# Performance work log

Hardware: AMD Instinct MI355X
Metric: run time of the kernel (lower is better)

## Reference

```python
import jax, jax.numpy as jnp
import numpy as np

B, S, H = 1, 4096, 2048
NH, HD = 16, 128
ROPE_N = 32
WINDOW = 1024
EPS = 1e-5


def _build_rope(seq_len, n_elem, base=10000.0):
    theta = 1.0 / (base ** (np.arange(0, n_elem, 2, dtype=np.float32) / n_elem))  # [n_elem/2]
    idx = np.arange(seq_len, dtype=np.float32)
    freqs = np.outer(idx, theta)                     # [S, n_elem/2]
    freqs = np.concatenate([freqs, freqs], axis=-1)  # [S, n_elem]
    return jnp.asarray(np.cos(freqs)), jnp.asarray(np.sin(freqs))


def setup_inputs() -> dict:
    key = jax.random.key(0)
    k1, k2, k3 = jax.random.split(key, 3)
    x = jax.random.normal(k1, (B, S, H), dtype=jnp.float32)
    cos, sin = _build_rope(S, ROPE_N)
    norm_weight = jnp.ones((H,), dtype=jnp.float32)
    qkv_w = jax.random.normal(k2, (3 * H, H), dtype=jnp.float32) * (1.0 / np.sqrt(H))
    o_w = jax.random.normal(k3, (H, H), dtype=jnp.float32) * (1.0 / np.sqrt(H))
    return {"x": x, "cos": cos, "sin": sin, "norm_weight": norm_weight,
            "qkv_w": qkv_w, "o_w": o_w}


def _apply_rope(t, cos, sin):
    # t: [B, NH, S, ROPE_N]; cos/sin: [S, ROPE_N]
    half = t.shape[-1] // 2
    x1, x2 = t[..., :half], t[..., half:]
    rotated = jnp.concatenate([-x2, x1], axis=-1)
    return t * cos + rotated * sin


def reference(x, cos, sin, norm_weight, qkv_w, o_w):
    b, s, h = x.shape
    # RMSNorm (computed in fp32)
    xf = x.astype(jnp.float32)
    ms = jnp.mean(xf * xf, axis=-1, keepdims=True)
    xn = (norm_weight * (xf * jax.lax.rsqrt(ms + EPS))).astype(x.dtype)
    # fused QKV projection
    qkv = jnp.einsum('bsh,oh->bso', xn, qkv_w)  # [B, S, 3H]
    q, k, v = jnp.split(qkv, 3, axis=-1)
    def to_heads(t):
        return t.reshape(b, s, NH, HD).transpose(0, 2, 1, 3)  # [B, NH, S, HD]
    q, k, v = to_heads(q), to_heads(k), to_heads(v)
    # partial RoPE on first ROPE_N dims
    q = jnp.concatenate([_apply_rope(q[..., :ROPE_N], cos, sin), q[..., ROPE_N:]], axis=-1)
    k = jnp.concatenate([_apply_rope(k[..., :ROPE_N], cos, sin), k[..., ROPE_N:]], axis=-1)
    # sliding-window causal attention: query i attends keys j with i-WINDOW <= j <= i
    scale = 1.0 / np.sqrt(HD)
    scores = jnp.einsum('bnqd,bnkd->bnqk', q, k) * scale  # [B, NH, S, S]
    i = jnp.arange(s)[:, None]
    j = jnp.arange(s)[None, :]
    mask = (j <= i) & (j >= i - WINDOW)
    scores = jnp.where(mask, scores, jnp.finfo(scores.dtype).min)
    attn = jax.nn.softmax(scores, axis=-1)
    out = jnp.einsum('bnqk,bnkd->bnqd', attn, v)  # [B, NH, S, HD]
    out = out.transpose(0, 2, 1, 3).reshape(b, s, h)
    return jnp.einsum('bsh,oh->bso', out, o_w)
```

## Files before the change

### kernel.cpp

```cpp
#include <hip/hip_runtime.h>
#include <stdint.h>

#define S_LEN 4096
#define HDIM  2048
#define NHEAD 16
#define HD    128
#define WIN   1024

typedef float  f32x4  __attribute__((ext_vector_type(4)));
typedef float  f32x4v __attribute__((ext_vector_type(4)));
typedef __bf16 bf16x8 __attribute__((ext_vector_type(8)));
typedef short  short8 __attribute__((ext_vector_type(8)));
typedef short  short4v __attribute__((ext_vector_type(4)));

static __device__ __forceinline__ short f2bf(float f) {
  union { float f; uint32_t u; } v; v.f = f;
  uint32_t r = (v.u + 0x7FFFu + ((v.u >> 16) & 1u)) >> 16;
  return (short)(uint16_t)r;
}

static __device__ __forceinline__ void gload_lds16(const void* g, void* l) {
  __builtin_amdgcn_global_load_lds((__attribute__((address_space(1))) void*)g,
                                   (__attribute__((address_space(3))) void*)l,
                                   16, 0, 0);
}

__global__ __launch_bounds__(256) void rmsnorm_k(const float* __restrict__ x,
                                                 const float* __restrict__ w,
                                                 short* __restrict__ xn) {
  const int row = blockIdx.x;
  const int t = threadIdx.x;
  const float* xr = x + (size_t)row * HDIM;
  f32x4v a = *(const f32x4v*)&xr[t * 8];
  f32x4v b = *(const f32x4v*)&xr[t * 8 + 4];
  float ss = a.x*a.x + a.y*a.y + a.z*a.z + a.w*a.w
           + b.x*b.x + b.y*b.y + b.z*b.z + b.w*b.w;
#pragma unroll
  for (int d = 1; d < 64; d <<= 1) ss += __shfl_xor(ss, d, 64);
  __shared__ float sred[4];
  if ((t & 63) == 0) sred[t >> 6] = ss;
  __syncthreads();
  float tot = sred[0] + sred[1] + sred[2] + sred[3];
  float rs = rsqrtf(tot * (1.0f / HDIM) + 1e-5f);
  float vv[8] = {a.x, a.y, a.z, a.w, b.x, b.y, b.z, b.w};
  const float* wp = w + t * 8;
  short8 o;
#pragma unroll
  for (int j = 0; j < 8; ++j) o[j] = f2bf(vv[j] * rs * wp[j]);
  *(short8*)&xn[(size_t)row * HDIM + t * 8] = o;
}

__global__ __launch_bounds__(256) void cvt_k(const float* __restrict__ in,
                                             short* __restrict__ out, int n4) {
  int i = blockIdx.x * 256 + threadIdx.x;
  if (i >= n4) return;
  f32x4v v = *(const f32x4v*)&in[(size_t)i * 4];
  short4v o = { f2bf(v.x), f2bf(v.y), f2bf(v.z), f2bf(v.w) };
  *(short4v*)&out[(size_t)i * 4] = o;
}

template <int EPI>
__global__ __launch_bounds__(256) void gemm_bt(
    const short* __restrict__ A, const short* __restrict__ Bt,
    int M, int N, int K, float* __restrict__ Cf,
    const float* __restrict__ cosb, const float* __restrict__ sinb,
    short* __restrict__ Qo, short* __restrict__ Ko, short* __restrict__ Vt) {
  __shared__ __align__(16) short Al[128 * 64];
  __shared__ __align__(16) short Bl[128 * 64];
  const int t = threadIdx.x;
  const int w = t >> 6, l = t & 63;
  const int lr = l & 15, lg = l >> 4;
  const int wr = w >> 1, wc = w & 1;
  const int brow = blockIdx.y * 128, bcol = blockIdx.x * 128;

  f32x4 acc[4][4] = {};

  const int srow = t >> 3;
  const int scol = (t & 7) * 8;
  const size_t abase = (size_t)(brow + srow) * K + scol;
  const size_t bbase = (size_t)(bcol + srow) * K + scol;

  for (int kt = 0; kt < K; kt += 64) {
#pragma unroll
    for (int i = 0; i < 4; ++i)
      gload_lds16(A + abase + (size_t)(i * 32) * K + kt, &Al[i * 2048 + w * 512]);
#pragma unroll
    for (int i = 0; i < 4; ++i)
      gload_lds16(Bt + bbase + (size_t)(i * 32) * K + kt, &Bl[i * 2048 + w * 512]);
    __syncthreads();
#pragma unroll
    for (int kk = 0; kk < 2; ++kk) {
      bf16x8 af[4], bfm[4];
#pragma unroll
      for (int m = 0; m < 4; ++m)
        af[m] = *(const bf16x8*)&Al[(wr * 64 + m * 16 + lr) * 64 + kk * 32 + lg * 8];
#pragma unroll
      for (int n = 0; n < 4; ++n)
        bfm[n] = *(const bf16x8*)&Bl[(wc * 64 + n * 16 + lr) * 64 + kk * 32 + lg * 8];
#pragma unroll
      for (int m = 0; m < 4; ++m)
#pragma unroll
        for (int n = 0; n < 4; ++n)
          acc[m][n] = __builtin_amdgcn_mfma_f32_16x16x32_bf16(af[m], bfm[n], acc[m][n], 0, 0, 0);
    }
    __syncthreads();
  }

  const int row0 = brow + wr * 64, col0 = bcol + wc * 64;
  if (EPI == 0) {
#pragma unroll
    for (int m = 0; m < 4; ++m)
#pragma unroll
      for (int n = 0; n < 4; ++n)
#pragma unroll
        for (int r = 0; r < 4; ++r)
          Cf[(size_t)(row0 + m * 16 + lg * 4 + r) * N + col0 + n * 16 + lr] = acc[m][n][r];
  } else {
    const int sec = col0 >> 11;
    const int headc = (col0 & 2047) >> 7;
    const bool rope = (sec < 2) && ((col0 & 127) == 0);
#pragma unroll
    for (int m = 0; m < 4; ++m) {
#pragma unroll
      for (int r = 0; r < 4; ++r) {
        const int s = row0 + m * 16 + lg * 4 + r;
        float v0 = acc[m][0][r], v1 = acc[m][1][r];
        float v2 = acc[m][2][r], v3 = acc[m][3][r];
        if (rope) {
          const int d0 = lr;
          float c0 = cosb[s * 32 + d0],      sn0 = sinb[s * 32 + d0];
          float c1 = cosb[s * 32 + d0 + 16], sn1 = sinb[s * 32 + d0 + 16];
          float t0 = v0 * c0 - v1 * sn0;
          float t1 = v1 * c1 + v0 * sn1;
          v0 = t0; v1 = t1;
        }
        float vv[4] = {v0, v1, v2, v3};
#pragma unroll
        for (int n = 0; n < 4; ++n) {
          const int col = col0 + n * 16 + lr;
          const int d = col & 127;
          if (sec == 0)
            Qo[((size_t)headc * S_LEN + s) * HD + d] = f2bf(vv[n] * 0.08838834764831845f);
          else if (sec == 1)
            Ko[((size_t)headc * S_LEN + s) * HD + d] = f2bf(vv[n]);
          else
            Vt[((size_t)headc * HD + d) * S_LEN + s] = f2bf(vv[n]);
        }
      }
    }
  }
}

__global__ __launch_bounds__(256) void attn_k(const short* __restrict__ Q,
                                              const short* __restrict__ Kk,
                                              const short* __restrict__ Vt,
                                              short* __restrict__ Ao) {
  __shared__ __align__(16) short Kl[64 * HD];
  __shared__ __align__(16) short Vl[HD * 64];
  __shared__ __align__(16) short Pl[4][16 * 72];
  const int head = blockIdx.y;
  int bxx = blockIdx.x;
  bxx = ((bxx & 7) << 3) | (bxx >> 3);
  const int qb = bxx * 64;
  const int w = threadIdx.x >> 6, l = threadIdx.x & 63;
  const int lr = l & 15, lg = l >> 4;
  const int q0w = qb + w * 16;
  const short* Qh = Q  + (size_t)head * S_LEN * HD;
  const short* Kh = Kk + (size_t)head * S_LEN * HD;
  const short* Vh = Vt + (size_t)head * HD * S_LEN;

  bf16x8 qf[4];
#pragma unroll
  for (int kk = 0; kk < 4; ++kk)
    qf[kk] = *(const bf16x8*)&Qh[(size_t)(q0w + lr) * HD + kk * 32 + lg * 8];

  f32x4 oacc[8] = {};
  float mrow[4], lrow[4];
#pragma unroll
  for (int r = 0; r < 4; ++r) { mrow[r] = -1e30f; lrow[r] = 0.0f; }

  const int k_begin = (qb >= WIN) ? (qb - WIN) : 0;
  const int nt = (qb + 64 - k_begin) >> 6;
  const int swz = (lr & 7) << 4;

  for (int tkv = 0; tkv < nt; ++tkv) {
    const int k0 = k_begin + tkv * 64;
#pragma unroll
    for (int i = 0; i < 4; ++i) {
      const int row = i * 16 + w * 4 + (l >> 4);
      gload_lds16(Kh + (size_t)(k0 + row) * HD + (((l & 15) ^ (row & 7)) * 8),
                  &Kl[(i * 16 + w * 4) * HD]);
    }
#pragma unroll
    for (int i = 0; i < 4; ++i) {
      const int row = i * 32 + w * 8 + (l >> 3);
      gload_lds16(Vh + (size_t)row * S_LEN + k0 + (((l & 7) ^ (row & 7)) * 8),
                  &Vl[(i * 32 + w * 8) * 64]);
    }
    __syncthreads();

    f32x4 sacc[4] = {};
#pragma unroll
    for (int nf = 0; nf < 4; ++nf) {
      const char* kb = (const char*)Kl + (nf * 16 + lr) * 256;
      bf16x8 kf[4];
#pragma unroll
      for (int kk = 0; kk < 4; ++kk)
        kf[kk] = *(const bf16x8*)(kb + ((kk * 64 + lg * 16) ^ swz));
#pragma unroll
      for (int kk = 0; kk < 4; ++kk)
        sacc[nf] = __builtin_amdgcn_mfma_f32_16x16x32_bf16(qf[kk], kf[nf == nf ? kk : kk], sacc[nf], 0, 0, 0);
    }

    const bool full = (k0 + 63 <= q0w) && (k0 >= q0w + 15 - WIN);
    float scl[4];
#pragma unroll
    for (int r = 0; r < 4; ++r) {
      const int i = q0w + lg * 4 + r;
      float sv[4];
#pragma unroll
      for (int nf = 0; nf < 4; ++nf) sv[nf] = sacc[nf][r];
      if (!full) {
#pragma unroll
        for (int nf = 0; nf < 4; ++nf) {
          const int j = k0 + nf * 16 + lr;
          if (!((j <= i) && (j + WIN >= i))) sv[nf] = -1e30f;
        }
      }
      float mx = fmaxf(fmaxf(sv[0], sv[1]), fmaxf(sv[2], sv[3]));
#pragma unroll
      for (int d = 1; d < 16; d <<= 1) mx = fmaxf(mx, __shfl_xor(mx, d, 64));
      const float mn = fmaxf(mrow[r], mx);
      const float sc = __expf(mrow[r] - mn);
      mrow[r] = mn;
      float p[4], rs = 0.0f;
#pragma unroll
      for (int nf = 0; nf < 4; ++nf) { p[nf] = __expf(sv[nf] - mn); rs += p[nf]; }
#pragma unroll
      for (int d = 1; d < 16; d <<= 1) rs += __shfl_xor(rs, d, 64);
      lrow[r] = lrow[r] * sc + rs;
      scl[r] = sc;
#pragma unroll
      for (int nf = 0; nf < 4; ++nf)
        Pl[w][(lg * 4 + r) * 72 + nf * 16 + lr] = f2bf(p[nf]);
    }
#pragma unroll
    for (int df = 0; df < 8; ++df)
#pragma unroll
      for (int r = 0; r < 4; ++r) oacc[df][r] *= scl[r];

    bf16x8 pa[2];
#pragma unroll
    for (int kk2 = 0; kk2 < 2; ++kk2)
      pa[kk2] = *(const bf16x8*)&Pl[w][lr * 72 + kk2 * 32 + lg * 8];

#pragma unroll
    for (int df = 0; df < 8; ++df) {
      const char* vb = (const char*)Vl + (df * 16 + lr) * 128;
#pragma unroll
      for (int kk2 = 0; kk2 < 2; ++kk2) {
        bf16x8 vfrag = *(const bf16x8*)(vb + ((kk2 * 64 + lg * 16) ^ swz));
        oacc[df] = __builtin_amdgcn_mfma_f32_16x16x32_bf16(pa[kk2], vfrag, oacc[df], 0, 0, 0);
      }
    }
    __syncthreads();
  }

  float inv[4];
#pragma unroll
  for (int r = 0; r < 4; ++r) inv[r] = 1.0f / lrow[r];
#pragma unroll
  for (int df = 0; df < 8; ++df)
#pragma unroll
    for (int r = 0; r < 4; ++r) {
      const int s = q0w + lg * 4 + r;
      Ao[(size_t)s * HDIM + head * HD + df * 16 + lr] = f2bf(oacc[df][r] * inv[r]);
    }
}

extern "C" void kernel_launch(void* const* d_in, const int* in_sizes, int n_in,
                              void* d_out, int out_size, void* d_ws, size_t ws_size,
                              hipStream_t stream) {
  const float* x    = (const float*)d_in[0];
  const float* cosb = (const float*)d_in[1];
  const float* sinb = (const float*)d_in[2];
  const float* nw   = (const float*)d_in[3];
  const float* qkvw = (const float*)d_in[4];
  const float* ow   = (const float*)d_in[5];
  float* out = (float*)d_out;

  short* ws = (short*)d_ws;
  short* xn = ws;
  short* wb = xn + (size_t)S_LEN * HDIM;
  short* Qb = wb + (size_t)3 * HDIM * HDIM;
  short* Kb = Qb + (size_t)NHEAD * S_LEN * HD;
  short* Vb = Kb + (size_t)NHEAD * S_LEN * HD;
  short* Ao = xn;

  rmsnorm_k<<<S_LEN, 256, 0, stream>>>(x, nw, xn);
  cvt_k<<<(3 * HDIM * HDIM / 4 + 255) / 256, 256, 0, stream>>>(qkvw, wb, 3 * HDIM * HDIM / 4);
  gemm_bt<1><<<dim3(3 * HDIM / 128, S_LEN / 128), 256, 0, stream>>>(
      xn, wb, S_LEN, 3 * HDIM, HDIM, nullptr, cosb, sinb, Qb, Kb, Vb);
  cvt_k<<<(HDIM * HDIM / 4 + 255) / 256, 256, 0, stream>>>(ow, wb, HDIM * HDIM / 4);
  attn_k<<<dim3(S_LEN / 64, NHEAD), 256, 0, stream>>>(Qb, Kb, Vb, Ao);
  gemm_bt<0><<<dim3(HDIM / 128, S_LEN / 128), 256, 0, stream>>>(
      Ao, wb, S_LEN, HDIM, HDIM, out, nullptr, nullptr, nullptr, nullptr, nullptr);
}
```

Measured before the change: 351.0 us.

## Rewrite GEMM with triple-buffered LDS pipeline, 256x128 tiles and XCD block remap

```diff
diff --git a/kernel.cpp b/kernel.cpp
--- a/kernel.cpp
+++ b/kernel.cpp
@@ -60,53 +60,101 @@
 }
 
 template <int EPI>
-__global__ __launch_bounds__(256) void gemm_bt(
+__global__ __launch_bounds__(512) void gemm_p(
     const short* __restrict__ A, const short* __restrict__ Bt,
     int M, int N, int K, float* __restrict__ Cf,
     const float* __restrict__ cosb, const float* __restrict__ sinb,
     short* __restrict__ Qo, short* __restrict__ Ko, short* __restrict__ Vt) {
-  __shared__ __align__(16) short Al[128 * 64];
-  __shared__ __align__(16) short Bl[128 * 64];
+  __shared__ __align__(16) short lds[3][24576];
   const int t = threadIdx.x;
-  const int w = t >> 6, l = t & 63;
+  const int wid = t >> 6, l = t & 63;
   const int lr = l & 15, lg = l >> 4;
-  const int wr = w >> 1, wc = w & 1;
-  const int brow = blockIdx.y * 128, bcol = blockIdx.x * 128;
+  const int wm = wid >> 1, wn = wid & 1;
+
+  int bid = blockIdx.x;
+  const int nwg = gridDim.x;
+  bid = (bid & 7) * (nwg >> 3) + (bid >> 3);
+  const int nbx = N >> 7;
+  const int bx = bid % nbx, by = bid / nbx;
+  const int brow = by * 256, bcol = bx * 128;
+
+  const int srow7 = (t >> 3) & 7;
+  const int scol = ((t & 7) ^ srow7) * 8;
 
   f32x4 acc[4][4] = {};
 
-  const int srow = t >> 3;
-  const int scol = (t & 7) * 8;
-  const size_t abase = (size_t)(brow + srow) * K + scol;
-  const size_t bbase = (size_t)(bcol + srow) * K + scol;
-
-  for (int kt = 0; kt < K; kt += 64) {
-#pragma unroll
-    for (int i = 0; i < 4; ++i)
-      gload_lds16(A + abase + (size_t)(i * 32) * K + kt, &Al[i * 2048 + w * 512]);
-#pragma unroll
-    for (int i = 0; i < 4; ++i)
-      gload_lds16(Bt + bbase + (size_t)(i * 32) * K + kt, &Bl[i * 2048 + w * 512]);
-    __syncthreads();
-#pragma unroll
-    for (int kk = 0; kk < 2; ++kk) {
-      bf16x8 af[4], bfm[4];
-#pragma unroll
-      for (int m = 0; m < 4; ++m)
-        af[m] = *(const bf16x8*)&Al[(wr * 64 + m * 16 + lr) * 64 + kk * 32 + lg * 8];
+  const int nt = K >> 6;
+
+#define STAGE_A(slot, kt, i)                                                     \
+  gload_lds16(A + (size_t)(brow + (i) * 64 + (t >> 3)) * K + (kt) + scol,        \
+              &lds[slot][(i) * 4096 + t * 8])
+#define STAGE_B(slot, kt, i)                                                     \
+  gload_lds16(Bt + (size_t)(bcol + (i) * 64 + (t >> 3)) * K + (kt) + scol,       \
+              &lds[slot][16384 + (i) * 4096 + t * 8])
+
+  STAGE_A(0, 0, 0); STAGE_A(0, 0, 1); STAGE_A(0, 0, 2); STAGE_A(0, 0, 3);
+  STAGE_B(0, 0, 0); STAGE_B(0, 0, 1);
+  STAGE_A(1, 64, 0); STAGE_A(1, 64, 1); STAGE_A(1, 64, 2); STAGE_A(1, 64, 3);
+  STAGE_B(1, 64, 0); STAGE_B(1, 64, 1);
+  asm volatile("s_waitcnt vmcnt(6)" ::: "memory");
+  __builtin_amdgcn_s_barrier();
+
+  const int xo0 = ((lg ^ (lr & 7)) << 3);
+  const int xo1 = (((4 + lg) ^ (lr & 7)) << 3);
+
+  int slot = 0;
+  for (int tt = 0; tt < nt; ++tt) {
+    const int s2 = (slot + 2 >= 3) ? slot - 1 : slot + 2;
+    const int kt2 = (tt + 2) << 6;
+    const bool st = (tt + 2 < nt);
+    bf16x8 af[4], bfr[4];
+
+#pragma unroll
+    for (int m = 0; m < 4; ++m)
+      af[m] = *(const bf16x8*)&lds[slot][(wm * 64 + m * 16 + lr) * 64 + xo0];
+#pragma unroll
+    for (int n = 0; n < 4; ++n)
+      bfr[n] = *(const bf16x8*)&lds[slot][16384 + (wn * 64 + n * 16 + lr) * 64 + xo0];
+    if (st) { STAGE_A(s2, kt2, 0); STAGE_A(s2, kt2, 1); STAGE_B(s2, kt2, 0); }
+    __builtin_amdgcn_s_barrier();
+    asm volatile("s_waitcnt lgkmcnt(0)" ::: "memory");
+    __builtin_amdgcn_sched_barrier(0);
+    __builtin_amdgcn_s_setprio(1);
+#pragma unroll
+    for (int m = 0; m < 4; ++m)
 #pragma unroll
       for (int n = 0; n < 4; ++n)
-        bfm[n] = *(const bf16x8*)&Bl[(wc * 64 + n * 16 + lr) * 64 + kk * 32 + lg * 8];
-#pragma unroll
-      for (int m = 0; m < 4; ++m)
-#pragma unroll
-        for (int n = 0; n < 4; ++n)
-          acc[m][n] = __builtin_amdgcn_mfma_f32_16x16x32_bf16(af[m], bfm[n], acc[m][n], 0, 0, 0);
-    }
-    __syncthreads();
+        acc[m][n] = __builtin_amdgcn_mfma_f32_16x16x32_bf16(af[m], bfr[n], acc[m][n], 0, 0, 0);
+    __builtin_amdgcn_s_setprio(0);
+    __builtin_amdgcn_s_barrier();
+
+#pragma unroll
+    for (int m = 0; m < 4; ++m)
+      af[m] = *(const bf16x8*)&lds[slot][(wm * 64 + m * 16 + lr) * 64 + xo1];
+#pragma unroll
+    for (int n = 0; n < 4; ++n)
+      bfr[n] = *(const bf16x8*)&lds[slot][16384 + (wn * 64 + n * 16 + lr) * 64 + xo1];
+    if (st) { STAGE_A(s2, kt2, 2); STAGE_A(s2, kt2, 3); STAGE_B(s2, kt2, 1); }
+    if (tt < nt - 2) asm volatile("s_waitcnt vmcnt(6)" ::: "memory");
+    else             asm volatile("s_waitcnt vmcnt(0)" ::: "memory");
+    __builtin_amdgcn_s_barrier();
+    asm volatile("s_waitcnt lgkmcnt(0)" ::: "memory");
+    __builtin_amdgcn_sched_barrier(0);
+    __builtin_amdgcn_s_setprio(1);
+#pragma unroll
+    for (int m = 0; m < 4; ++m)
+#pragma unroll
+      for (int n = 0; n < 4; ++n)
+        acc[m][n] = __builtin_amdgcn_mfma_f32_16x16x32_bf16(af[m], bfr[n], acc[m][n], 0, 0, 0);
+    __builtin_amdgcn_s_setprio(0);
+    __builtin_amdgcn_s_barrier();
+
+    slot = (slot + 1 >= 3) ? 0 : slot + 1;
   }
-
-  const int row0 = brow + wr * 64, col0 = bcol + wc * 64;
+#undef STAGE_A
+#undef STAGE_B
+
+  const int row0 = brow + wm * 64, col0 = bcol + wn * 64;
   if (EPI == 0) {
 #pragma unroll
     for (int m = 0; m < 4; ++m)
@@ -209,7 +257,7 @@
         kf[kk] = *(const bf16x8*)(kb + ((kk * 64 + lg * 16) ^ swz));
 #pragma unroll
       for (int kk = 0; kk < 4; ++kk)
-        sacc[nf] = __builtin_amdgcn_mfma_f32_16x16x32_bf16(qf[kk], kf[nf == nf ? kk : kk], sacc[nf], 0, 0, 0);
+        sacc[nf] = __builtin_amdgcn_mfma_f32_16x16x32_bf16(qf[kk], kf[kk], sacc[nf], 0, 0, 0);
     }
 
     const bool full = (k0 + 63 <= q0w) && (k0 >= q0w + 15 - WIN);
@@ -299,10 +347,10 @@
 
   rmsnorm_k<<<S_LEN, 256, 0, stream>>>(x, nw, xn);
   cvt_k<<<(3 * HDIM * HDIM / 4 + 255) / 256, 256, 0, stream>>>(qkvw, wb, 3 * HDIM * HDIM / 4);
-  gemm_bt<1><<<dim3(3 * HDIM / 128, S_LEN / 128), 256, 0, stream>>>(
+  gemm_p<1><<<(3 * HDIM / 128) * (S_LEN / 256), 512, 0, stream>>>(
       xn, wb, S_LEN, 3 * HDIM, HDIM, nullptr, cosb, sinb, Qb, Kb, Vb);
   cvt_k<<<(HDIM * HDIM / 4 + 255) / 256, 256, 0, stream>>>(ow, wb, HDIM * HDIM / 4);
   attn_k<<<dim3(S_LEN / 64, NHEAD), 256, 0, stream>>>(Qb, Kb, Vb, Ao);
-  gemm_bt<0><<<dim3(HDIM / 128, S_LEN / 128), 256, 0, stream>>>(
+  gemm_p<0><<<(HDIM / 128) * (S_LEN / 256), 512, 0, stream>>>(
       Ao, wb, S_LEN, HDIM, HDIM, out, nullptr, nullptr, nullptr, nullptr, nullptr);
 }
```

New measurement: 307.1 us. 1.14x faster.

## Rewrite GEMM as 256x256-tile, 512-thread kernel with 4-stage async LDS pipeline

Applied to the files above, without the earlier changes.

```diff
diff --git a/kernel.cpp b/kernel.cpp
--- a/kernel.cpp
+++ b/kernel.cpp
@@ -60,56 +60,78 @@
 }
 
 template <int EPI>
-__global__ __launch_bounds__(256) void gemm_bt(
+__global__ __launch_bounds__(512, 2) void gemm_p2(
     const short* __restrict__ A, const short* __restrict__ Bt,
     int M, int N, int K, float* __restrict__ Cf,
     const float* __restrict__ cosb, const float* __restrict__ sinb,
     short* __restrict__ Qo, short* __restrict__ Ko, short* __restrict__ Vt) {
-  __shared__ __align__(16) short Al[128 * 64];
-  __shared__ __align__(16) short Bl[128 * 64];
+  __shared__ __align__(16) short lds[4][16384];
   const int t = threadIdx.x;
   const int w = t >> 6, l = t & 63;
   const int lr = l & 15, lg = l >> 4;
-  const int wr = w >> 1, wc = w & 1;
-  const int brow = blockIdx.y * 128, bcol = blockIdx.x * 128;
-
-  f32x4 acc[4][4] = {};
-
-  const int srow = t >> 3;
-  const int scol = (t & 7) * 8;
-  const size_t abase = (size_t)(brow + srow) * K + scol;
-  const size_t bbase = (size_t)(bcol + srow) * K + scol;
-
-  for (int kt = 0; kt < K; kt += 64) {
-#pragma unroll
-    for (int i = 0; i < 4; ++i)
-      gload_lds16(A + abase + (size_t)(i * 32) * K + kt, &Al[i * 2048 + w * 512]);
-#pragma unroll
-    for (int i = 0; i < 4; ++i)
-      gload_lds16(Bt + bbase + (size_t)(i * 32) * K + kt, &Bl[i * 2048 + w * 512]);
-    __syncthreads();
-#pragma unroll
-    for (int kk = 0; kk < 2; ++kk) {
-      bf16x8 af[4], bfm[4];
-#pragma unroll
-      for (int m = 0; m < 4; ++m)
-        af[m] = *(const bf16x8*)&Al[(wr * 64 + m * 16 + lr) * 64 + kk * 32 + lg * 8];
+  const int wm = w >> 2, wn = w & 3;
+
+  int bid = blockIdx.x;
+  const int nwg = gridDim.x;
+  bid = (bid & 7) * (nwg >> 3) + (bid >> 3);
+  const int nby = M >> 8;
+  const int by = bid % nby, bx = bid / nby;
+  const int brow = by * 256, bcol = bx * 256;
+
+  const int srow_l = l >> 2;
+  const int scol = (((l & 3) ^ ((l >> 3) & 3)) * 8);
+
+  f32x4 acc[8][4] = {};
+  const int nt = K >> 5;
+
+#define STAGE_A(s, kt, j)                                                      \
+  gload_lds16(A + (size_t)(brow + (j) * 128 + w * 16 + srow_l) * K + (kt) + scol, \
+              &lds[s][(j) * 4096 + w * 512])
+#define STAGE_B(s, kt, j)                                                      \
+  gload_lds16(Bt + (size_t)(bcol + (j) * 128 + w * 16 + srow_l) * K + (kt) + scol, \
+              &lds[s][8192 + (j) * 4096 + w * 512])
+#define STAGE(s, kt) do { STAGE_A(s, kt, 0); STAGE_A(s, kt, 1);                \
+                          STAGE_B(s, kt, 0); STAGE_B(s, kt, 1); } while (0)
+
+  STAGE(0, 0); STAGE(1, 32); STAGE(2, 64);
+
+  const int xoff = ((lg ^ ((lr >> 1) & 3)) << 4);
+  const int arow = (wm * 128 + lr) * 64;
+  const int brow_b = 16384 + (wn * 64 + lr) * 64;
+
+  for (int tt = 0; tt < nt; ++tt) {
+    if (tt < nt - 2)       asm volatile("s_waitcnt vmcnt(8)" ::: "memory");
+    else if (tt == nt - 2) asm volatile("s_waitcnt vmcnt(4)" ::: "memory");
+    else                   asm volatile("s_waitcnt vmcnt(0)" ::: "memory");
+    __builtin_amdgcn_s_barrier();
+    __builtin_amdgcn_sched_barrier(0);
+    const int slot = tt & 3;
+    if (tt + 3 < nt) STAGE((tt + 3) & 3, (tt + 3) << 5);
+
+    const char* sb = (const char*)&lds[slot][0];
+    bf16x8 af[8], bfr[4];
+#pragma unroll
+    for (int m = 0; m < 8; ++m)
+      af[m] = *(const bf16x8*)(sb + arow + m * 1024 + xoff);
+#pragma unroll
+    for (int n = 0; n < 4; ++n)
+      bfr[n] = *(const bf16x8*)(sb + brow_b + n * 1024 + xoff);
+    __builtin_amdgcn_s_setprio(1);
+#pragma unroll
+    for (int m = 0; m < 8; ++m)
 #pragma unroll
       for (int n = 0; n < 4; ++n)
-        bfm[n] = *(const bf16x8*)&Bl[(wc * 64 + n * 16 + lr) * 64 + kk * 32 + lg * 8];
-#pragma unroll
-      for (int m = 0; m < 4; ++m)
-#pragma unroll
-        for (int n = 0; n < 4; ++n)
-          acc[m][n] = __builtin_amdgcn_mfma_f32_16x16x32_bf16(af[m], bfm[n], acc[m][n], 0, 0, 0);
-    }
-    __syncthreads();
+        acc[m][n] = __builtin_amdgcn_mfma_f32_16x16x32_bf16(af[m], bfr[n], acc[m][n], 0, 0, 0);
+    __builtin_amdgcn_s_setprio(0);
   }
-
-  const int row0 = brow + wr * 64, col0 = bcol + wc * 64;
+#undef STAGE
+#undef STAGE_A
+#undef STAGE_B
+
+  const int row0 = brow + wm * 128, col0 = bcol + wn * 64;
   if (EPI == 0) {
 #pragma unroll
-    for (int m = 0; m < 4; ++m)
+    for (int m = 0; m < 8; ++m)
 #pragma unroll
       for (int n = 0; n < 4; ++n)
 #pragma unroll
@@ -120,7 +142,7 @@
     const int headc = (col0 & 2047) >> 7;
     const bool rope = (sec < 2) && ((col0 & 127) == 0);
 #pragma unroll
-    for (int m = 0; m < 4; ++m) {
+    for (int m = 0; m < 8; ++m) {
 #pragma unroll
       for (int r = 0; r < 4; ++r) {
         const int s = row0 + m * 16 + lg * 4 + r;
@@ -209,7 +231,7 @@
         kf[kk] = *(const bf16x8*)(kb + ((kk * 64 + lg * 16) ^ swz));
 #pragma unroll
       for (int kk = 0; kk < 4; ++kk)
-        sacc[nf] = __builtin_amdgcn_mfma_f32_16x16x32_bf16(qf[kk], kf[nf == nf ? kk : kk], sacc[nf], 0, 0, 0);
+        sacc[nf] = __builtin_amdgcn_mfma_f32_16x16x32_bf16(qf[kk], kf[kk], sacc[nf], 0, 0, 0);
     }
 
     const bool full = (k0 + 63 <= q0w) && (k0 >= q0w + 15 - WIN);
@@ -299,10 +321,10 @@
 
   rmsnorm_k<<<S_LEN, 256, 0, stream>>>(x, nw, xn);
   cvt_k<<<(3 * HDIM * HDIM / 4 + 255) / 256, 256, 0, stream>>>(qkvw, wb, 3 * HDIM * HDIM / 4);
-  gemm_bt<1><<<dim3(3 * HDIM / 128, S_LEN / 128), 256, 0, stream>>>(
+  gemm_p2<1><<<(3 * HDIM / 256) * (S_LEN / 256), 512, 0, stream>>>(
       xn, wb, S_LEN, 3 * HDIM, HDIM, nullptr, cosb, sinb, Qb, Kb, Vb);
   cvt_k<<<(HDIM * HDIM / 4 + 255) / 256, 256, 0, stream>>>(ow, wb, HDIM * HDIM / 4);
   attn_k<<<dim3(S_LEN / 64, NHEAD), 256, 0, stream>>>(Qb, Kb, Vb, Ao);
-  gemm_bt<0><<<dim3(HDIM / 128, S_LEN / 128), 256, 0, stream>>>(
+  gemm_p2<0><<<(HDIM / 256) * (S_LEN / 256), 512, 0, stream>>>(
       Ao, wb, S_LEN, HDIM, HDIM, out, nullptr, nullptr, nullptr, nullptr, nullptr);
 }
```

New measurement: 348.4 us. About the same (-0.8%).

## Rewrite GEMM as 256x128 tile with double-buffered software-pipelined LDS loads

Applied to the files above, without the earlier changes.

```diff
diff --git a/kernel.cpp b/kernel.cpp
--- a/kernel.cpp
+++ b/kernel.cpp
@@ -59,54 +59,90 @@
   *(short4v*)&out[(size_t)i * 4] = o;
 }
 
+
+template <int D, int KH>
+__device__ __forceinline__ void ph_compute(const short* ldsb, f32x4 (&acc)[4][4],
+                                           int aro, int bro) {
+  const short* pl = ldsb + D * 24576;
+  bf16x8 af[4], bfr[4];
+#pragma unroll
+  for (int m = 0; m < 4; ++m)
+    af[m] = *(const bf16x8*)&pl[KH * 8192 + aro + m * 512];
+#pragma unroll
+  for (int n = 0; n < 4; ++n)
+    bfr[n] = *(const bf16x8*)&pl[16384 + KH * 4096 + bro + n * 512];
+  __builtin_amdgcn_s_setprio(1);
+#pragma unroll
+  for (int m = 0; m < 4; ++m)
+#pragma unroll
+    for (int n = 0; n < 4; ++n)
+      acc[m][n] = __builtin_amdgcn_mfma_f32_16x16x32_bf16(af[m], bfr[n], acc[m][n], 0, 0, 0);
+  __builtin_amdgcn_s_setprio(0);
+}
+
 template <int EPI>
-__global__ __launch_bounds__(256) void gemm_bt(
+__global__ __launch_bounds__(512, 2) void gemm_p3(
     const short* __restrict__ A, const short* __restrict__ Bt,
     int M, int N, int K, float* __restrict__ Cf,
     const float* __restrict__ cosb, const float* __restrict__ sinb,
     short* __restrict__ Qo, short* __restrict__ Ko, short* __restrict__ Vt) {
-  __shared__ __align__(16) short Al[128 * 64];
-  __shared__ __align__(16) short Bl[128 * 64];
+  __shared__ __align__(16) short lds[2][24576];
   const int t = threadIdx.x;
   const int w = t >> 6, l = t & 63;
   const int lr = l & 15, lg = l >> 4;
-  const int wr = w >> 1, wc = w & 1;
-  const int brow = blockIdx.y * 128, bcol = blockIdx.x * 128;
+  const int wm = w >> 1, wn = w & 1;
+
+  int bid = blockIdx.x;
+  const int nwg = gridDim.x;
+  bid = (bid & 7) * (nwg >> 3) + (bid >> 3);
+  const int nby = M >> 8;
+  const int by = bid % nby, bx = bid / nby;
+  const int brow = by * 256, bcol = bx * 128;
+
+  const int srow = t >> 2;
+  const int sg = (t & 3) ^ ((srow + (srow >> 2)) & 3);
+  const short* As0 = A  + (size_t)(brow + srow) * K + sg * 8;
+  const short* As1 = A  + (size_t)(brow + 128 + srow) * K + sg * 8;
+  const short* Bs  = Bt + (size_t)(bcol + srow) * K + sg * 8;
+
+  const int fr = (lr + (lr >> 2)) & 3;
+  const int aro = (wm * 64 + lr) * 32 + ((lg ^ fr) * 8);
+  const int bro = (wn * 64 + lr) * 32 + ((lg ^ fr) * 8);
 
   f32x4 acc[4][4] = {};
-
-  const int srow = t >> 3;
-  const int scol = (t & 7) * 8;
-  const size_t abase = (size_t)(brow + srow) * K + scol;
-  const size_t bbase = (size_t)(bcol + srow) * K + scol;
-
-  for (int kt = 0; kt < K; kt += 64) {
-#pragma unroll
-    for (int i = 0; i < 4; ++i)
-      gload_lds16(A + abase + (size_t)(i * 32) * K + kt, &Al[i * 2048 + w * 512]);
-#pragma unroll
-    for (int i = 0; i < 4; ++i)
-      gload_lds16(Bt + bbase + (size_t)(i * 32) * K + kt, &Bl[i * 2048 + w * 512]);
-    __syncthreads();
-#pragma unroll
-    for (int kk = 0; kk < 2; ++kk) {
-      bf16x8 af[4], bfm[4];
-#pragma unroll
-      for (int m = 0; m < 4; ++m)
-        af[m] = *(const bf16x8*)&Al[(wr * 64 + m * 16 + lr) * 64 + kk * 32 + lg * 8];
-#pragma unroll
-      for (int n = 0; n < 4; ++n)
-        bfm[n] = *(const bf16x8*)&Bl[(wc * 64 + n * 16 + lr) * 64 + kk * 32 + lg * 8];
-#pragma unroll
-      for (int m = 0; m < 4; ++m)
-#pragma unroll
-        for (int n = 0; n < 4; ++n)
-          acc[m][n] = __builtin_amdgcn_mfma_f32_16x16x32_bf16(af[m], bfm[n], acc[m][n], 0, 0, 0);
-    }
-    __syncthreads();
+  const int nt = K >> 6;
+  const short* ldsb = &lds[0][0];
+
+#define STG(SD, U, SKH) do {                                             \
+    const size_t ko = (size_t)((U) * 64 + (SKH) * 32);                   \
+    gload_lds16(As0 + ko, &lds[SD][(SKH) * 8192 + t * 8]);               \
+    gload_lds16(As1 + ko, &lds[SD][(SKH) * 8192 + 4096 + t * 8]);        \
+    gload_lds16(Bs  + ko, &lds[SD][16384 + (SKH) * 4096 + t * 8]);       \
+  } while (0)
+
+#define PHASE(D, KH, VM, DOSTG, SD, SU, SKH)                             \
+  asm volatile("s_waitcnt vmcnt(" #VM ")" ::: "memory");                 \
+  __builtin_amdgcn_s_barrier();                                          \
+  __builtin_amdgcn_sched_barrier(0);                                     \
+  if (DOSTG) { STG(SD, SU, SKH); }                                       \
+  ph_compute<D, KH>(ldsb, acc, aro, bro);
+
+  STG(0, 0, 0); STG(0, 0, 1); STG(1, 1, 0);
+
+  for (int u = 0; u < nt - 2; u += 2) {
+    PHASE(0, 0, 6, true, 1, u + 1, 1)
+    PHASE(0, 1, 6, true, 0, u + 2, 0)
+    PHASE(1, 0, 6, true, 0, u + 2, 1)
+    PHASE(1, 1, 6, true, 1, u + 3, 0)
   }
-
-  const int row0 = brow + wr * 64, col0 = bcol + wc * 64;
+  PHASE(0, 0, 6, true, 1, nt - 1, 1)
+  PHASE(0, 1, 6, false, 0, 0, 0)
+  PHASE(1, 0, 3, false, 0, 0, 0)
+  PHASE(1, 1, 0, false, 0, 0, 0)
+#undef PHASE
+#undef STG
+
+  const int row0 = brow + wm * 64, col0 = bcol + wn * 64;
   if (EPI == 0) {
 #pragma unroll
     for (int m = 0; m < 4; ++m)
@@ -209,7 +245,7 @@
         kf[kk] = *(const bf16x8*)(kb + ((kk * 64 + lg * 16) ^ swz));
 #pragma unroll
       for (int kk = 0; kk < 4; ++kk)
-        sacc[nf] = __builtin_amdgcn_mfma_f32_16x16x32_bf16(qf[kk], kf[nf == nf ? kk : kk], sacc[nf], 0, 0, 0);
+        sacc[nf] = __builtin_amdgcn_mfma_f32_16x16x32_bf16(qf[kk], kf[kk], sacc[nf], 0, 0, 0);
     }
 
     const bool full = (k0 + 63 <= q0w) && (k0 >= q0w + 15 - WIN);
@@ -299,10 +335,10 @@
 
   rmsnorm_k<<<S_LEN, 256, 0, stream>>>(x, nw, xn);
   cvt_k<<<(3 * HDIM * HDIM / 4 + 255) / 256, 256, 0, stream>>>(qkvw, wb, 3 * HDIM * HDIM / 4);
-  gemm_bt<1><<<dim3(3 * HDIM / 128, S_LEN / 128), 256, 0, stream>>>(
+  gemm_p3<1><<<(S_LEN / 256) * (3 * HDIM / 128), 512, 0, stream>>>(
       xn, wb, S_LEN, 3 * HDIM, HDIM, nullptr, cosb, sinb, Qb, Kb, Vb);
   cvt_k<<<(HDIM * HDIM / 4 + 255) / 256, 256, 0, stream>>>(ow, wb, HDIM * HDIM / 4);
   attn_k<<<dim3(S_LEN / 64, NHEAD), 256, 0, stream>>>(Qb, Kb, Vb, Ao);
-  gemm_bt<0><<<dim3(HDIM / 128, S_LEN / 128), 256, 0, stream>>>(
+  gemm_p3<0><<<(S_LEN / 256) * (HDIM / 128), 512, 0, stream>>>(
       Ao, wb, S_LEN, HDIM, HDIM, out, nullptr, nullptr, nullptr, nullptr, nullptr);
 }
```

Result: faster. 318.7 us (-9.2%).
